# Performance work log

Hardware: AMD Instinct MI355X
Metric: run time of the kernel (lower is better)

## Reference

```python
import jax, jax.numpy as jnp
import numpy as np

G, NPG = 2048, 512          # glimpses, points per glimpse
N0 = G * NPG                # 1,048,576 input points
CPG, CPG2 = 128, 32         # clusters per glimpse at level1/level2
M1, M2 = G * CPG, G * CPG2  # 262144, 65536


def _seg_mean_np(x, ids, m):
    cnt = np.bincount(ids, minlength=m).astype(np.float32)
    out = np.stack([np.bincount(ids, weights=x[:, d], minlength=m) for d in range(x.shape[1])], axis=1)
    return (out / np.maximum(cnt, 1.0)[:, None]).astype(np.float32)


def setup_inputs() -> dict:
    key = jax.random.key(0)
    ks = jax.random.split(key, 16)
    rng = np.random.default_rng(0)
    pos_np = (rng.random((N0, 3)) * 4.0).astype(np.float32)
    # voxel_mean_pool level 0: each point -> a cluster within its glimpse
    g_of_pt = np.arange(N0) // NPG
    out_index0 = (g_of_pt * CPG + rng.integers(0, CPG, N0)).astype(np.int64)
    pos1_np = _seg_mean_np(pos_np, out_index0, M1)
    g_of_c1 = np.arange(M1) // CPG
    out_index1 = (g_of_c1 * CPG2 + rng.integers(0, CPG2, M1)).astype(np.int64)
    pos2_np = _seg_mean_np(pos1_np, out_index1, M2)
    out_index2 = (np.arange(M2) // CPG2).astype(np.int64)  # glimpse id per level-2 point

    def w(k, shp, s=0.05):
        return jax.random.normal(k, shp, dtype=jnp.float32) * s

    return {
        "rgb": jax.random.normal(ks[0], (N0, 1), dtype=jnp.float32),
        "pos": jnp.asarray(pos_np), "pos1": jnp.asarray(pos1_np), "pos2": jnp.asarray(pos2_np),
        "out_index0": jnp.asarray(out_index0), "out_index1": jnp.asarray(out_index1),
        "out_index2": jnp.asarray(out_index2),
        "eps": jax.random.normal(ks[1], (G, 128), dtype=jnp.float32),
        # conv1: local (c_in=1 + 3 -> 16), global (16 -> 32)
        "W1l": w(ks[2], (4, 16)), "b1l": jnp.zeros(16), "W1g": w(ks[3], (16, 32)), "b1g": jnp.zeros(32),
        # conv2: (32+3 -> 64), (64 -> 128)
        "W2l": w(ks[4], (35, 64)), "b2l": jnp.zeros(64), "W2g": w(ks[5], (64, 128)), "b2g": jnp.zeros(128),
        # conv3: (128+3 -> 128), (128 -> 256)
        "W3l": w(ks[6], (131, 128)), "b3l": jnp.zeros(128), "W3g": w(ks[7], (128, 256)), "b3g": jnp.zeros(256),
        "Wlin": w(ks[8], (256, 256)), "blin": jnp.zeros(256),
    }


def _point_conv(x_in, pos_in, pos_out, out_index, Wl, bl, Wg, bg):
    # gather relative position of each input point w.r.t. its output center
    rel = pos_in - pos_out[out_index]                      # [E,3]
    h = jax.nn.celu(jnp.concatenate([x_in, rel], -1) @ Wl + bl)  # per-edge MLP
    m = pos_out.shape[0]
    cnt = jax.ops.segment_sum(jnp.ones((h.shape[0],), h.dtype), out_index, num_segments=m)
    agg = jax.ops.segment_sum(h, out_index, num_segments=m) / jnp.maximum(cnt, 1.0)[:, None]
    return agg @ Wg + bg


def reference(rgb, pos, pos1, pos2, out_index0, out_index1, out_index2, eps,
              W1l, b1l, W1g, b1g, W2l, b2l, W2g, b2g, W3l, b3l, W3g, b3g, Wlin, blin):
    f = rgb  # ar=False path: feature = rgb
    f = jax.nn.celu(_point_conv(f, pos, pos1, out_index0, W1l, b1l, W1g, b1g))   # [M1,32]
    f = jax.nn.celu(_point_conv(f, pos1, pos2, out_index1, W2l, b2l, W2g, b2g))  # [M2,128]
    centers = jnp.zeros((G, 3), f.dtype)  # pos_sample = zeros_like(glimpse__center)
    f = jax.nn.celu(_point_conv(f, pos2, centers, out_index2, W3l, b3l, W3g, b3g))  # [G,256]
    out = f @ Wlin + blin
    mu, sg = jnp.split(out, 2, axis=1)
    sigma = jax.nn.softplus(sg)  # to_sigma
    z = mu + sigma * eps         # Normal.rsample
    z_what, z_mask = jnp.split(z, 2, axis=1)
    return z_what, z_mask, mu, sigma, f
```

## Files before the change

kernel.cpp:

```cpp
#include <hip/hip_runtime.h>
#include <hip/hip_bf16.h>
#include <cstddef>

#define G_   2048
#define NPG_ 512
#define CPG_ 128
#define CPG2_ 32
#define N0_  (G_*NPG_)
#define M1_  (G_*CPG_)
#define M2_  (G_*CPG2_)

#define OFF_ZW 0
#define OFF_ZM (G_*64)
#define OFF_MU (2*G_*64)
#define OFF_SG (2*G_*64 + G_*128)
#define OFF_F  (2*G_*64 + 2*G_*128)

typedef __attribute__((ext_vector_type(8))) short bf16x8;
typedef __attribute__((ext_vector_type(4))) float f32x4;

__device__ __forceinline__ float celu_f(float x)     { return x > 0.f ? x : __expf(x) - 1.f; }
__device__ __forceinline__ float softplus_f(float x) { return fmaxf(x, 0.f) + __logf(1.f + __expf(-fabsf(x))); }
__device__ __forceinline__ unsigned short f2bf(float x) {
    __hip_bfloat16 h = __float2bfloat16(x);
    return *reinterpret_cast<unsigned short*>(&h);
}

__global__ void k_prep(const float* __restrict__ W2l, const float* __restrict__ W2g,
                       const float* __restrict__ W3l,
                       unsigned short* __restrict__ w2lT, unsigned short* __restrict__ w2gT,
                       unsigned short* __restrict__ w3lT)
{
    const int tid = blockIdx.x*256 + threadIdx.x, stride = gridDim.x*256;
    for (int i = tid; i < 64*64; i += stride) {
        const int ch = i >> 6, k = i & 63;
        w2lT[i] = f2bf(k < 35 ? W2l[k*64 + ch] : 0.f);
    }
    for (int i = tid; i < 128*64; i += stride) {
        const int ch = i >> 6, k = i & 63;
        w2gT[i] = f2bf(W2g[k*128 + ch]);
    }
    for (int i = tid; i < 128*160; i += stride) {
        const int ch = i / 160, k = i % 160;
        w3lT[i] = f2bf(k < 131 ? W3l[k*128 + ch] : 0.f);
    }
}

__global__ __launch_bounds__(256, 6) void k_conv1(
    const float* __restrict__ rgb, const float* __restrict__ pos, const float* __restrict__ pos1,
    const int* __restrict__ idx0, const float* __restrict__ W1l, const float* __restrict__ b1l,
    const float* __restrict__ W1g, const float* __restrict__ b1g, unsigned short* __restrict__ f1)
{
    const int g = blockIdx.x, t = threadIdx.x;
    __shared__ float sx0[NPG_], srx[NPG_], sry[NPG_], srz[NPG_];
    __shared__ unsigned short slc1[NPG_], order[NPG_];
    __shared__ int cnt[CPG_], start[CPG_], ctr[CPG_], scan[CPG_];
    __shared__ float aggT[CPG_*20];
    __shared__ float sW1g[512];

    for (int i = t; i < 512; i += 256) sW1g[i] = W1g[i];
    if (t < CPG_) cnt[t] = 0;
    __syncthreads();

    #pragma unroll
    for (int r = 0; r < 2; r++) {
        const int lp = r*256 + t;
        const int p  = g*NPG_ + lp;
        const int c  = idx0[p];
        const int lc = c - g*CPG_;
        sx0[lp] = rgb[p];
        srx[lp] = pos[p*3+0] - pos1[c*3+0];
        sry[lp] = pos[p*3+1] - pos1[c*3+1];
        srz[lp] = pos[p*3+2] - pos1[c*3+2];
        slc1[lp] = (unsigned short)lc;
        atomicAdd(&cnt[lc], 1);
    }
    __syncthreads();

    if (t < CPG_) scan[t] = cnt[t];
    __syncthreads();
    #pragma unroll
    for (int d = 1; d < CPG_; d <<= 1) {
        int v = 0;
        if (t < CPG_ && t >= d) v = scan[t - d];
        __syncthreads();
        if (t < CPG_) scan[t] += v;
        __syncthreads();
    }
    if (t < CPG_) { const int s = scan[t] - cnt[t]; start[t] = s; ctr[t] = s; }
    __syncthreads();

    #pragma unroll
    for (int r = 0; r < 2; r++) {
        const int lp = r*256 + t;
        const int slot = atomicAdd(&ctr[slc1[lp]], 1);
        order[slot] = (unsigned short)lp;
    }
    __syncthreads();

    {
        const int c = t >> 1, ch0 = (t & 1) * 8;
        float wj[8], wx[8], wy[8], wz[8], bb2[8];
        #pragma unroll
        for (int j = 0; j < 8; j++) {
            wj[j] = W1l[ch0+j]; wx[j] = W1l[16+ch0+j];
            wy[j] = W1l[32+ch0+j]; wz[j] = W1l[48+ch0+j];
            bb2[j] = b1l[ch0+j];
        }
        float a[8];
        #pragma unroll
        for (int j = 0; j < 8; j++) a[j] = 0.f;
        const int n = cnt[c], base = start[c];
        for (int i = 0; i < n; i++) {
            const int lp = order[base + i];
            const float x0 = sx0[lp], rx = srx[lp], ry = sry[lp], rz = srz[lp];
            #pragma unroll
            for (int j = 0; j < 8; j++) {
                const float h = bb2[j] + x0*wj[j] + rx*wx[j] + ry*wy[j] + rz*wz[j];
                a[j] += celu_f(h);
            }
        }
        const float inv = 1.f / fmaxf((float)n, 1.f);
        #pragma unroll
        for (int j = 0; j < 8; j++) aggT[c*20 + ch0 + j] = a[j] * inv;
    }
    __syncthreads();

    const int oc = t & 31;
    float wreg[16];
    #pragma unroll
    for (int j = 0; j < 16; j++) wreg[j] = sW1g[j*32 + oc];
    const float bg = b1g[oc];
    #pragma unroll
    for (int i = 0; i < 16; i++) {
        const int lc = (t >> 5) + i*8;
        float a = bg;
        #pragma unroll
        for (int j = 0; j < 16; j += 4) {
            const float4 a4 = *(const float4*)&aggT[lc*20 + j];
            a += a4.x*wreg[j] + a4.y*wreg[j+1] + a4.z*wreg[j+2] + a4.w*wreg[j+3];
        }
        f1[(size_t)(g*CPG_ + lc)*32 + oc] = f2bf(celu_f(a));
    }
}

__global__ __launch_bounds__(256, 5) void k_conv2(
    const unsigned short* __restrict__ f1, const float* __restrict__ pos1, const float* __restrict__ pos2,
    const int* __restrict__ idx1, const unsigned short* __restrict__ w2lT, const float* __restrict__ b2l,
    const unsigned short* __restrict__ w2gT, const float* __restrict__ b2g, unsigned short* __restrict__ f2)
{
    const int g = blockIdx.x, t = threadIdx.x;
    const int lane = t & 63, wv = t >> 6;
    const int lr = lane & 15, quad = lane >> 4;
    __shared__ __align__(16) unsigned short xs16[CPG_*72];
    __shared__ __align__(16) unsigned short sT[32*136];
    __shared__ int   slc[CPG_];
    __shared__ int   cnti[CPG2_];
    __shared__ float invc[CPG2_];
    unsigned short* const HT   = xs16;
    unsigned short* const agg2 = sT;

    for (int i = t; i < 1088; i += 256) ((uint2*)sT)[i] = make_uint2(0u, 0u);
    if (t < CPG2_) cnti[t] = 0;
    {
        const uint4 v0 = ((const uint4*)f1)[(size_t)g*512 + t*2];
        const uint4 v1 = ((const uint4*)f1)[(size_t)g*512 + t*2 + 1];
        const int row = t >> 1, col = (t & 1) * 16;
        *(uint4*)&xs16[row*72 + col]     = v0;
        *(uint4*)&xs16[row*72 + col + 8] = v1;
    }
    for (int i = t; i < 128*29; i += 256) {
        const int r = i / 29, c = 35 + (i - r*29);
        xs16[r*72 + c] = 0;
    }
    if (t < CPG_) {
        const int c2 = idx1[g*CPG_ + t];
        slc[t] = c2 - g*CPG2_;
        #pragma unroll
        for (int d = 0; d < 3; d++)
            xs16[t*72 + 32 + d] = f2bf(pos1[(g*CPG_ + t)*3 + d] - pos2[c2*3 + d]);
    }
    __syncthreads();

    float hv[8][4];
    {
        const int chn = wv*16 + lr;
        const bf16x8 bw0 = *(const bf16x8*)&w2lT[chn*64 + quad*8];
        const bf16x8 bw1 = *(const bf16x8*)&w2lT[chn*64 + 32 + quad*8];
        const float bias = b2l[chn];
        #pragma unroll
        for (int m = 0; m < 8; m++) {
            f32x4 acc = (f32x4){bias, bias, bias, bias};
            const bf16x8 a0 = *(const bf16x8*)&xs16[(m*16 + lr)*72 + quad*8];
            const bf16x8 a1 = *(const bf16x8*)&xs16[(m*16 + lr)*72 + 32 + quad*8];
            acc = __builtin_amdgcn_mfma_f32_16x16x32_bf16(a0, bw0, acc, 0, 0, 0);
            acc = __builtin_amdgcn_mfma_f32_16x16x32_bf16(a1, bw1, acc, 0, 0, 0);
            #pragma unroll
            for (int r = 0; r < 4; r++) hv[m][r] = celu_f(acc[r]);
        }
    }
    if (t < CPG_) {
        sT[slc[t]*136 + t] = 0x3F80;
        atomicAdd(&cnti[slc[t]], 1);
    }
    __syncthreads();

    {
        const int chn = wv*16 + lr;
        #pragma unroll
        for (int m = 0; m < 8; m++) {
            uint2 p;
            p.x = (unsigned)f2bf(hv[m][0]) | ((unsigned)f2bf(hv[m][1]) << 16);
            p.y = (unsigned)f2bf(hv[m][2]) | ((unsigned)f2bf(hv[m][3]) << 16);
            *(uint2*)&HT[chn*136 + m*16 + quad*4] = p;
        }
    }
    if (t < CPG2_) invc[t] = 1.f / fmaxf((float)cnti[t], 1.f);
    __syncthreads();

    float aggv[2][4];
    {
        const int ch = wv*16 + lr;
        f32x4 acc[2];
        acc[0] = (f32x4){0.f, 0.f, 0.f, 0.f};
        acc[1] = (f32x4){0.f, 0.f, 0.f, 0.f};
        #pragma unroll
        for (int ks = 0; ks < 4; ks++) {
            const bf16x8 b = *(const bf16x8*)&HT[ch*136 + ks*32 + quad*8];
            #pragma unroll
            for (int mt = 0; mt < 2; mt++) {
                const bf16x8 a = *(const bf16x8*)&sT[(mt*16 + lr)*136 + ks*32 + quad*8];
                acc[mt] = __builtin_amdgcn_mfma_f32_16x16x32_bf16(a, b, acc[mt], 0, 0, 0);
            }
        }
        #pragma unroll
        for (int mt = 0; mt < 2; mt++)
        #pragma unroll
        for (int r = 0; r < 4; r++) {
            const int s = mt*16 + quad*4 + r;
            aggv[mt][r] = acc[mt][r] * invc[s];
        }
    }
    __syncthreads();

    {
        const int ch = wv*16 + lr;
        #pragma unroll
        for (int mt = 0; mt < 2; mt++)
        #pragma unroll
        for (int r = 0; r < 4; r++)
            agg2[(mt*16 + quad*4 + r)*72 + ch] = f2bf(aggv[mt][r]);
    }
    __syncthreads();

    {
        f32x4 acc2[2][2];
        int   chn2[2];
        bf16x8 bw[2][2];
        #pragma unroll
        for (int nt = 0; nt < 2; nt++) {
            chn2[nt] = (wv + nt*4)*16 + lr;
            const float bias = b2g[chn2[nt]];
            #pragma unroll
            for (int mt = 0; mt < 2; mt++) acc2[nt][mt] = (f32x4){bias, bias, bias, bias};
            bw[nt][0] = *(const bf16x8*)&w2gT[chn2[nt]*64 + quad*8];
            bw[nt][1] = *(const bf16x8*)&w2gT[chn2[nt]*64 + 32 + quad*8];
        }
        #pragma unroll
        for (int ks = 0; ks < 2; ks++) {
            #pragma unroll
            for (int mt = 0; mt < 2; mt++) {
                const bf16x8 a = *(const bf16x8*)&agg2[(mt*16 + lr)*72 + ks*32 + quad*8];
                acc2[0][mt] = __builtin_amdgcn_mfma_f32_16x16x32_bf16(a, bw[0][ks], acc2[0][mt], 0, 0, 0);
                acc2[1][mt] = __builtin_amdgcn_mfma_f32_16x16x32_bf16(a, bw[1][ks], acc2[1][mt], 0, 0, 0);
            }
        }
        #pragma unroll
        for (int nt = 0; nt < 2; nt++)
        #pragma unroll
        for (int mt = 0; mt < 2; mt++)
        #pragma unroll
        for (int r = 0; r < 4; r++) {
            const int row = mt*16 + quad*4 + r;
            f2[(size_t)(g*CPG2_ + row)*128 + chn2[nt]] = f2bf(celu_f(acc2[nt][mt][r]));
        }
    }
}

__global__ __launch_bounds__(256, 4) void k_conv3(
    const unsigned short* __restrict__ f2, const float* __restrict__ pos2,
    const unsigned short* __restrict__ w3lT, const float* __restrict__ b3l,
    const float* __restrict__ W3g, const float* __restrict__ b3g,
    const float* __restrict__ Wlin, const float* __restrict__ blin,
    const float* __restrict__ eps, float* __restrict__ out)
{
    const int g0 = blockIdx.x * 2, t = threadIdx.x;
    const int lane = t & 63, wv = t >> 6;
    const int lr = lane & 15, quad = lane >> 4;
    __shared__ __align__(16) unsigned short xs16[64*168];
    __shared__ float red2[2*128*9];
    __shared__ float agg[256];
    __shared__ float f3s[512];
    __shared__ float outs[512];

    {
        const int row = t >> 2, q = t & 3;
        const size_t base = (size_t)(g0*CPG2_ + row)*16 + q*4;
        const uint4 v0 = ((const uint4*)f2)[base + 0];
        const uint4 v1 = ((const uint4*)f2)[base + 1];
        const uint4 v2 = ((const uint4*)f2)[base + 2];
        const uint4 v3 = ((const uint4*)f2)[base + 3];
        *(uint4*)&xs16[row*168 + q*32]      = v0;
        *(uint4*)&xs16[row*168 + q*32 + 8]  = v1;
        *(uint4*)&xs16[row*168 + q*32 + 16] = v2;
        *(uint4*)&xs16[row*168 + q*32 + 24] = v3;
    }
    for (int i = t; i < 64*29; i += 256) {
        const int r = i / 29, c = 131 + (i - r*29);
        xs16[r*168 + c] = 0;
    }
    if (t < 64) {
        #pragma unroll
        for (int d = 0; d < 3; d++)
            xs16[t*168 + 128 + d] = f2bf(pos2[(g0*CPG2_ + t)*3 + d]);
    }
    __syncthreads();

    {
        f32x4 acc[2][4];
        int chn[2];
        #pragma unroll
        for (int nt = 0; nt < 2; nt++) {
            chn[nt] = (wv + nt*4)*16 + lr;
            const float bias = b3l[chn[nt]];
            #pragma unroll
            for (int mt = 0; mt < 4; mt++) acc[nt][mt] = (f32x4){bias, bias, bias, bias};
        }
        #pragma unroll
        for (int ks = 0; ks < 5; ks++) {
            const bf16x8 b0 = *(const bf16x8*)&w3lT[chn[0]*160 + ks*32 + quad*8];
            const bf16x8 b1 = *(const bf16x8*)&w3lT[chn[1]*160 + ks*32 + quad*8];
            #pragma unroll
            for (int mt = 0; mt < 4; mt++) {
                const bf16x8 a = *(const bf16x8*)&xs16[(mt*16 + lr)*168 + ks*32 + quad*8];
                acc[0][mt] = __builtin_amdgcn_mfma_f32_16x16x32_bf16(a, b0, acc[0][mt], 0, 0, 0);
                acc[1][mt] = __builtin_amdgcn_mfma_f32_16x16x32_bf16(a, b1, acc[1][mt], 0, 0, 0);
            }
        }
        #pragma unroll
        for (int nt = 0; nt < 2; nt++)
        #pragma unroll
        for (int mt = 0; mt < 4; mt++) {
            float p = celu_f(acc[nt][mt][0]) + celu_f(acc[nt][mt][1])
                    + celu_f(acc[nt][mt][2]) + celu_f(acc[nt][mt][3]);
            const int gl = mt >> 1, pidx = (mt & 1)*4 + quad;
            red2[(gl*128 + chn[nt])*9 + pidx] = p;
        }
    }
    __syncthreads();
    {
        const int gl = t >> 7, ch = t & 127;
        const float* rp = &red2[(gl*128 + ch)*9];
        float a = 0.f;
        #pragma unroll
        for (int p = 0; p < 8; p++) a += rp[p];
        agg[gl*128 + ch] = a * (1.f/32.f);
    }
    __syncthreads();

    {
        float a0 = b3g[t], a1 = a0;
        #pragma unroll 2
        for (int k = 0; k < 128; k += 4) {
            const float4 ga = *(const float4*)&agg[k];
            const float4 gb = *(const float4*)&agg[128 + k];
            const float w0 = W3g[(k+0)*256+t], w1 = W3g[(k+1)*256+t];
            const float w2 = W3g[(k+2)*256+t], w3 = W3g[(k+3)*256+t];
            a0 += ga.x*w0 + ga.y*w1 + ga.z*w2 + ga.w*w3;
            a1 += gb.x*w0 + gb.y*w1 + gb.z*w2 + gb.w*w3;
        }
        f3s[t]       = celu_f(a0);
        f3s[256 + t] = celu_f(a1);
    }
    __syncthreads();

    {
        float a0 = blin[t], a1 = a0;
        #pragma unroll 2
        for (int k = 0; k < 256; k += 4) {
            const float4 fa = *(const float4*)&f3s[k];
            const float4 fb = *(const float4*)&f3s[256 + k];
            const float w0 = Wlin[(k+0)*256+t], w1 = Wlin[(k+1)*256+t];
            const float w2 = Wlin[(k+2)*256+t], w3 = Wlin[(k+3)*256+t];
            a0 += fa.x*w0 + fa.y*w1 + fa.z*w2 + fa.w*w3;
            a1 += fb.x*w0 + fb.y*w1 + fb.z*w2 + fb.w*w3;
        }
        outs[t]       = a0;
        outs[256 + t] = a1;
    }
    out[OFF_F + (size_t)g0*256 + t]     = f3s[t];
    out[OFF_F + (size_t)(g0+1)*256 + t] = f3s[256 + t];
    __syncthreads();

    if (t < 128) {
        #pragma unroll
        for (int gl = 0; gl < 2; gl++) {
            const int g = g0 + gl;
            const float mu    = outs[gl*256 + t];
            const float sigma = softplus_f(outs[gl*256 + 128 + t]);
            const float z     = mu + sigma * eps[g*128 + t];
            out[OFF_MU + g*128 + t] = mu;
            out[OFF_SG + g*128 + t] = sigma;
            if (t < 64) out[OFF_ZW + g*64 + t] = z;
            else        out[OFF_ZM + g*64 + (t - 64)] = z;
        }
    }
}

extern "C" void kernel_launch(void* const* d_in, const int* in_sizes, int n_in,
                              void* d_out, int out_size, void* d_ws, size_t ws_size,
                              hipStream_t stream)
{
    const float* rgb  = (const float*)d_in[0];
    const float* pos  = (const float*)d_in[1];
    const float* pos1 = (const float*)d_in[2];
    const float* pos2 = (const float*)d_in[3];
    const int*   idx0 = (const int*)d_in[4];
    const int*   idx1 = (const int*)d_in[5];
    const float* eps  = (const float*)d_in[7];
    const float* W1l = (const float*)d_in[8],  *b1l = (const float*)d_in[9];
    const float* W1g = (const float*)d_in[10], *b1g = (const float*)d_in[11];
    const float* W2l = (const float*)d_in[12], *b2l = (const float*)d_in[13];
    const float* W2g = (const float*)d_in[14], *b2g = (const float*)d_in[15];
    const float* W3l = (const float*)d_in[16], *b3l = (const float*)d_in[17];
    const float* W3g = (const float*)d_in[18], *b3g = (const float*)d_in[19];
    const float* Wlin = (const float*)d_in[20], *blin = (const float*)d_in[21];

    unsigned short* f1   = (unsigned short*)d_ws;
    unsigned short* f2   = f1 + (size_t)M1_*32;
    unsigned short* w2lT = f2 + (size_t)M2_*128;
    unsigned short* w2gT = w2lT + 64*64;
    unsigned short* w3lT = w2gT + 128*64;
    float* outp = (float*)d_out;

    k_prep <<<32,   256, 0, stream>>>(W2l, W2g, W3l, w2lT, w2gT, w3lT);
    k_conv1<<<G_,   256, 0, stream>>>(rgb, pos, pos1, idx0, W1l, b1l, W1g, b1g, f1);
    k_conv2<<<G_,   256, 0, stream>>>(f1, pos1, pos2, idx1, w2lT, b2l, w2gT, b2g, f2);
    k_conv3<<<G_/2, 256, 0, stream>>>(f2, pos2, w3lT, b3l, W3g, b3g, Wlin, blin, eps, outp);
}
```

Before: 174.0 us.

## Fold weight prep into conv1, use MFMA for conv3 dense layers, shuffle scan

The separate weight-transpose kernel is removed and its work is folded into k_conv1 as a grid-stride prologue. That prologue now also produces bf16 transposed copies of W3g and Wlin. k_conv3 replaces its scalar fp32 FMA loops for the global MLP and the final linear layer with bf16 MFMA 16x16x32 tiles, padding the two-glimpse rows to 16 with zeros. The shared-memory prefix scan in conv1 becomes a wavefront shuffle scan to cut barriers. In exchange the last two matmuls run in lower precision, most MFMA rows are wasted padding, and the conv2 HT alias edit is cosmetic.

```diff
diff --git a/kernel.cpp b/kernel.cpp
--- a/kernel.cpp
+++ b/kernel.cpp
@@ -26,32 +26,42 @@
     return *reinterpret_cast<unsigned short*>(&h);
 }
 
-__global__ void k_prep(const float* __restrict__ W2l, const float* __restrict__ W2g,
-                       const float* __restrict__ W3l,
-                       unsigned short* __restrict__ w2lT, unsigned short* __restrict__ w2gT,
-                       unsigned short* __restrict__ w3lT)
-{
-    const int tid = blockIdx.x*256 + threadIdx.x, stride = gridDim.x*256;
-    for (int i = tid; i < 64*64; i += stride) {
-        const int ch = i >> 6, k = i & 63;
-        w2lT[i] = f2bf(k < 35 ? W2l[k*64 + ch] : 0.f);
-    }
-    for (int i = tid; i < 128*64; i += stride) {
-        const int ch = i >> 6, k = i & 63;
-        w2gT[i] = f2bf(W2g[k*128 + ch]);
-    }
-    for (int i = tid; i < 128*160; i += stride) {
-        const int ch = i / 160, k = i % 160;
-        w3lT[i] = f2bf(k < 131 ? W3l[k*128 + ch] : 0.f);
-    }
-}
-
 __global__ __launch_bounds__(256, 6) void k_conv1(
     const float* __restrict__ rgb, const float* __restrict__ pos, const float* __restrict__ pos1,
     const int* __restrict__ idx0, const float* __restrict__ W1l, const float* __restrict__ b1l,
-    const float* __restrict__ W1g, const float* __restrict__ b1g, unsigned short* __restrict__ f1)
+    const float* __restrict__ W1g, const float* __restrict__ b1g, unsigned short* __restrict__ f1,
+    const float* __restrict__ W2l, const float* __restrict__ W2g, const float* __restrict__ W3l,
+    const float* __restrict__ W3g, const float* __restrict__ Wlin,
+    unsigned short* __restrict__ w2lT, unsigned short* __restrict__ w2gT,
+    unsigned short* __restrict__ w3lT, unsigned short* __restrict__ w3gT,
+    unsigned short* __restrict__ wlinT)
 {
     const int g = blockIdx.x, t = threadIdx.x;
+
+    {
+        const size_t tid = (size_t)g*256 + t, stride = (size_t)gridDim.x*256;
+        for (size_t i = tid; i < 64*64; i += stride) {
+            const int ch = i >> 6, k = i & 63;
+            w2lT[i] = f2bf(k < 35 ? W2l[k*64 + ch] : 0.f);
+        }
+        for (size_t i = tid; i < 128*64; i += stride) {
+            const int ch = i >> 6, k = i & 63;
+            w2gT[i] = f2bf(W2g[k*128 + ch]);
+        }
+        for (size_t i = tid; i < 128*160; i += stride) {
+            const int ch = i / 160, k = i % 160;
+            w3lT[i] = f2bf(k < 131 ? W3l[k*128 + ch] : 0.f);
+        }
+        for (size_t i = tid; i < 256*128; i += stride) {
+            const int ch = i >> 7, k = i & 127;
+            w3gT[i] = f2bf(W3g[k*256 + ch]);
+        }
+        for (size_t i = tid; i < 256*256; i += stride) {
+            const int ch = i >> 8, k = i & 255;
+            wlinT[i] = f2bf(Wlin[k*256 + ch]);
+        }
+    }
+
     __shared__ float sx0[NPG_], srx[NPG_], sry[NPG_], srz[NPG_];
     __shared__ unsigned short slc1[NPG_], order[NPG_];
     __shared__ int cnt[CPG_], start[CPG_], ctr[CPG_], scan[CPG_];
@@ -77,16 +87,19 @@
     }
     __syncthreads();
 
-    if (t < CPG_) scan[t] = cnt[t];
-    __syncthreads();
-    #pragma unroll
-    for (int d = 1; d < CPG_; d <<= 1) {
-        int v = 0;
-        if (t < CPG_ && t >= d) v = scan[t - d];
-        __syncthreads();
-        if (t < CPG_) scan[t] += v;
-        __syncthreads();
-    }
+    if (t < CPG_) {
+        int val = cnt[t];
+        const int ln = t & 63;
+        #pragma unroll
+        for (int d = 1; d < 64; d <<= 1) {
+            const int v = __shfl_up(val, d, 64);
+            if (ln >= d) val += v;
+        }
+        scan[t] = val;
+    }
+    __syncthreads();
+    if (t >= 64 && t < CPG_) scan[t] += scan[63];
+    __syncthreads();
     if (t < CPG_) { const int s = scan[t] - cnt[t]; start[t] = s; ctr[t] = s; }
     __syncthreads();
 
@@ -157,7 +170,8 @@
     __shared__ int   slc[CPG_];
     __shared__ int   cnti[CPG2_];
     __shared__ float invc[CPG2_];
-    unsigned short* const HT   = xs16;
+    unsigned short* const HT   = sT - 0 + 0, *const HT_unused = nullptr;
+    unsigned short* const HTp  = xs16;
     unsigned short* const agg2 = sT;
 
     for (int i = t; i < 1088; i += 256) ((uint2*)sT)[i] = make_uint2(0u, 0u);
@@ -212,7 +226,7 @@
             uint2 p;
             p.x = (unsigned)f2bf(hv[m][0]) | ((unsigned)f2bf(hv[m][1]) << 16);
             p.y = (unsigned)f2bf(hv[m][2]) | ((unsigned)f2bf(hv[m][3]) << 16);
-            *(uint2*)&HT[chn*136 + m*16 + quad*4] = p;
+            *(uint2*)&HTp[chn*136 + m*16 + quad*4] = p;
         }
     }
     if (t < CPG2_) invc[t] = 1.f / fmaxf((float)cnti[t], 1.f);
@@ -226,7 +240,7 @@
         acc[1] = (f32x4){0.f, 0.f, 0.f, 0.f};
         #pragma unroll
         for (int ks = 0; ks < 4; ks++) {
-            const bf16x8 b = *(const bf16x8*)&HT[ch*136 + ks*32 + quad*8];
+            const bf16x8 b = *(const bf16x8*)&HTp[ch*136 + ks*32 + quad*8];
             #pragma unroll
             for (int mt = 0; mt < 2; mt++) {
                 const bf16x8 a = *(const bf16x8*)&sT[(mt*16 + lr)*136 + ks*32 + quad*8];
@@ -290,19 +304,20 @@
 __global__ __launch_bounds__(256, 4) void k_conv3(
     const unsigned short* __restrict__ f2, const float* __restrict__ pos2,
     const unsigned short* __restrict__ w3lT, const float* __restrict__ b3l,
-    const float* __restrict__ W3g, const float* __restrict__ b3g,
-    const float* __restrict__ Wlin, const float* __restrict__ blin,
+    const unsigned short* __restrict__ w3gT, const float* __restrict__ b3g,
+    const unsigned short* __restrict__ wlinT, const float* __restrict__ blin,
     const float* __restrict__ eps, float* __restrict__ out)
 {
     const int g0 = blockIdx.x * 2, t = threadIdx.x;
     const int lane = t & 63, wv = t >> 6;
     const int lr = lane & 15, quad = lane >> 4;
     __shared__ __align__(16) unsigned short xs16[64*168];
-    __shared__ float red2[2*128*9];
-    __shared__ float agg[256];
-    __shared__ float f3s[512];
+    __shared__ __align__(16) float red2[2*128*9];
+    __shared__ __align__(16) unsigned short aggB[16*136];
     __shared__ float outs[512];
-
+    unsigned short* const f3B = (unsigned short*)red2;
+
+    for (int i = t; i < 1088; i += 256) ((unsigned*)aggB)[i] = 0u;
     {
         const int row = t >> 2, q = t & 3;
         const size_t base = (size_t)(g0*CPG2_ + row)*16 + q*4;
@@ -358,48 +373,77 @@
         }
     }
     __syncthreads();
-    {
+
+    if (t < 256) {
         const int gl = t >> 7, ch = t & 127;
         const float* rp = &red2[(gl*128 + ch)*9];
         float a = 0.f;
         #pragma unroll
         for (int p = 0; p < 8; p++) a += rp[p];
-        agg[gl*128 + ch] = a * (1.f/32.f);
-    }
-    __syncthreads();
-
-    {
-        float a0 = b3g[t], a1 = a0;
-        #pragma unroll 2
-        for (int k = 0; k < 128; k += 4) {
-            const float4 ga = *(const float4*)&agg[k];
-            const float4 gb = *(const float4*)&agg[128 + k];
-            const float w0 = W3g[(k+0)*256+t], w1 = W3g[(k+1)*256+t];
-            const float w2 = W3g[(k+2)*256+t], w3 = W3g[(k+3)*256+t];
-            a0 += ga.x*w0 + ga.y*w1 + ga.z*w2 + ga.w*w3;
-            a1 += gb.x*w0 + gb.y*w1 + gb.z*w2 + gb.w*w3;
-        }
-        f3s[t]       = celu_f(a0);
-        f3s[256 + t] = celu_f(a1);
-    }
-    __syncthreads();
-
-    {
-        float a0 = blin[t], a1 = a0;
-        #pragma unroll 2
-        for (int k = 0; k < 256; k += 4) {
-            const float4 fa = *(const float4*)&f3s[k];
-            const float4 fb = *(const float4*)&f3s[256 + k];
-            const float w0 = Wlin[(k+0)*256+t], w1 = Wlin[(k+1)*256+t];
-            const float w2 = Wlin[(k+2)*256+t], w3 = Wlin[(k+3)*256+t];
-            a0 += fa.x*w0 + fa.y*w1 + fa.z*w2 + fa.w*w3;
-            a1 += fb.x*w0 + fb.y*w1 + fb.z*w2 + fb.w*w3;
-        }
-        outs[t]       = a0;
-        outs[256 + t] = a1;
-    }
-    out[OFF_F + (size_t)g0*256 + t]     = f3s[t];
-    out[OFF_F + (size_t)(g0+1)*256 + t] = f3s[256 + t];
+        aggB[gl*136 + ch] = f2bf(a * (1.f/32.f));
+    }
+    __syncthreads();
+
+    for (int i = t; i < 14*264; i += 256) f3B[2*264 + i] = 0;
+
+    {
+        f32x4 c3[4];
+        int ch3[4];
+        #pragma unroll
+        for (int nt = 0; nt < 4; nt++) {
+            ch3[nt] = (wv + nt*4)*16 + lr;
+            const float bias = b3g[ch3[nt]];
+            c3[nt] = (f32x4){bias, bias, bias, bias};
+        }
+        #pragma unroll
+        for (int ks = 0; ks < 4; ks++) {
+            const bf16x8 a = *(const bf16x8*)&aggB[lr*136 + ks*32 + quad*8];
+            #pragma unroll
+            for (int nt = 0; nt < 4; nt++) {
+                const bf16x8 b = *(const bf16x8*)&w3gT[ch3[nt]*128 + ks*32 + quad*8];
+                c3[nt] = __builtin_amdgcn_mfma_f32_16x16x32_bf16(a, b, c3[nt], 0, 0, 0);
+            }
+        }
+        if (quad == 0) {
+            #pragma unroll
+            for (int nt = 0; nt < 4; nt++) {
+                const float v0 = celu_f(c3[nt][0]);
+                const float v1 = celu_f(c3[nt][1]);
+                out[OFF_F + (size_t)g0*256 + ch3[nt]]     = v0;
+                out[OFF_F + (size_t)(g0+1)*256 + ch3[nt]] = v1;
+                f3B[ch3[nt]]       = f2bf(v0);
+                f3B[264 + ch3[nt]] = f2bf(v1);
+            }
+        }
+    }
+    __syncthreads();
+
+    {
+        f32x4 cl[4];
+        int ch4[4];
+        #pragma unroll
+        for (int nt = 0; nt < 4; nt++) {
+            ch4[nt] = (wv + nt*4)*16 + lr;
+            const float bias = blin[ch4[nt]];
+            cl[nt] = (f32x4){bias, bias, bias, bias};
+        }
+        #pragma unroll
+        for (int ks = 0; ks < 8; ks++) {
+            const bf16x8 a = *(const bf16x8*)&f3B[lr*264 + ks*32 + quad*8];
+            #pragma unroll
+            for (int nt = 0; nt < 4; nt++) {
+                const bf16x8 b = *(const bf16x8*)&wlinT[ch4[nt]*256 + ks*32 + quad*8];
+                cl[nt] = __builtin_amdgcn_mfma_f32_16x16x32_bf16(a, b, cl[nt], 0, 0, 0);
+            }
+        }
+        if (quad == 0) {
+            #pragma unroll
+            for (int nt = 0; nt < 4; nt++) {
+                outs[ch4[nt]]       = cl[nt][0];
+                outs[256 + ch4[nt]] = cl[nt][1];
+            }
+        }
+    }
     __syncthreads();
 
     if (t < 128) {
@@ -436,15 +480,18 @@
     const float* W3g = (const float*)d_in[18], *b3g = (const float*)d_in[19];
     const float* Wlin = (const float*)d_in[20], *blin = (const float*)d_in[21];
 
-    unsigned short* f1   = (unsigned short*)d_ws;
-    unsigned short* f2   = f1 + (size_t)M1_*32;
-    unsigned short* w2lT = f2 + (size_t)M2_*128;
-    unsigned short* w2gT = w2lT + 64*64;
-    unsigned short* w3lT = w2gT + 128*64;
+    unsigned short* f1    = (unsigned short*)d_ws;
+    unsigned short* f2    = f1 + (size_t)M1_*32;
+    unsigned short* w2lT  = f2 + (size_t)M2_*128;
+    unsigned short* w2gT  = w2lT + 64*64;
+    unsigned short* w3lT  = w2gT + 128*64;
+    unsigned short* w3gT  = w3lT + 128*160;
+    unsigned short* wlinT = w3gT + 256*128;
     float* outp = (float*)d_out;
 
-    k_prep <<<32,   256, 0, stream>>>(W2l, W2g, W3l, w2lT, w2gT, w3lT);
-    k_conv1<<<G_,   256, 0, stream>>>(rgb, pos, pos1, idx0, W1l, b1l, W1g, b1g, f1);
+    k_conv1<<<G_,   256, 0, stream>>>(rgb, pos, pos1, idx0, W1l, b1l, W1g, b1g, f1,
+                                      W2l, W2g, W3l, W3g, Wlin,
+                                      w2lT, w2gT, w3lT, w3gT, wlinT);
     k_conv2<<<G_,   256, 0, stream>>>(f1, pos1, pos2, idx1, w2lT, b2l, w2gT, b2g, f2);
-    k_conv3<<<G_/2, 256, 0, stream>>>(f2, pos2, w3lT, b3l, W3g, b3g, Wlin, blin, eps, outp);
+    k_conv3<<<G_/2, 256, 0, stream>>>(f2, pos2, w3lT, b3l, w3gT, b3g, wlinT, blin, eps, outp);
 }
```

Result: no change. 177.3 us (+1.9%).
